# Kernel optimization log

Hardware: AMD Instinct MI355X
Metric: run time of the kernel (lower is better)

Reference implementation:

```python
import jax, jax.numpy as jnp
import numpy as np

B = 8192      # batch
D = 512       # ode state dim = 4*h_dim
U = 100       # ode net hidden units
K_STEPS = 20  # opt.ode1_step
EPS = 0.01    # opt.ode2_eps


def setup_inputs() -> dict:
    key = jax.random.key(0)
    ks = jax.random.split(key, 12)
    std = 0.1  # init_network_weights std
    return {
        "y0": jax.random.normal(ks[0], (B, D), jnp.float32),
        "t_seq": jax.random.uniform(ks[1], (B, 2), dtype=jnp.float32),
        "W1": std * jax.random.normal(ks[2], (U, D), jnp.float32),
        "b1": jnp.zeros((U,), jnp.float32),
        "W2": std * jax.random.normal(ks[3], (U, U), jnp.float32),
        "b2": jnp.zeros((U,), jnp.float32),
        "W3": std * jax.random.normal(ks[4], (D, U), jnp.float32),
        "b3": jnp.zeros((D,), jnp.float32),
        "b_phi_zt": jax.random.normal(ks[5], (B, 1), jnp.float32),
        # derivative of Nonpositive net is <= 0; log(-b' + 0.01) requires b' < 0.01
        "b_phi_zt_deriv": -jax.random.uniform(ks[6], (B, 1), dtype=jnp.float32),
        "s_phi_zt": jax.random.normal(ks[7], (B, 1), jnp.float32),
        "s_phi_zt_deriv": jax.random.uniform(ks[8], (B, 1), dtype=jnp.float32),
        "k": K_STEPS,
    }


def _ode_net(y, W1, b1, W2, b2, W3, b3):
    # create_net(D, D, n_layers=1, n_units=U): Linear->Tanh->Linear->Tanh->Linear
    h = jnp.tanh(y @ W1.T + b1)
    h = jnp.tanh(h @ W2.T + b2)
    return h @ W3.T + b3


def _forward(y0, t_seq, W1, b1, W2, b2, W3, b3,
             b_phi_zt, b_phi_zt_deriv, s_phi_zt, s_phi_zt_deriv, k):
    # ---- DiffeqSolver: k fixed Euler steps, gradient net ignores t ----
    dt = (t_seq[:, 1:2] - t_seq[:, 0:1]) / k  # [B,1]

    def euler_step(yi, _):
        yi = yi + _ode_net(yi, W1, b1, W2, b2, W3, b3) * dt
        return yi, None

    y_final, _ = jax.lax.scan(euler_step, y0, None, length=k)

    # ---- DiffeqSolver_KL: y_t = y0 + eps * cumsum(g(m_t)); y0 = 0 ----
    const = 0.01
    Kv = s_phi_zt + jnp.log(-b_phi_zt_deriv + const) - jnp.log(s_phi_zt_deriv + const)  # [B,1]
    T = int(round(1.0 / EPS)) - 1  # steps t = 1 .. int(1/eps)-1
    ms = (-1.0 + EPS * jnp.arange(1, T + 1, dtype=jnp.float32))[:, None, None]  # [T,1,1]
    log_neg_m = jnp.log(-ms)
    gm = -b_phi_zt_deriv / (ms * log_neg_m) * (Kv - jnp.log(-log_neg_m))  # [T,B,1]
    ycum = EPS * jnp.cumsum(gm, axis=0)  # solutions[t-1] = ycum[t-1]
    loss = ycum[-1] + (ycum[-2] - ycum[-1])  # first_item + Gm_eps  -> [B,1]

    return jnp.concatenate([y_final, loss], axis=-1)  # [B, D+1]


def reference(y0, t_seq, W1, b1, W2, b2, W3, b3,
              b_phi_zt, b_phi_zt_deriv, s_phi_zt, s_phi_zt_deriv, k):
    return _forward(y0, t_seq, W1, b1, W2, b2, W3, b3,
                    b_phi_zt, b_phi_zt_deriv, s_phi_zt, s_phi_zt_deriv, k)
```

## Files before the change

kernel.cpp:

```cpp
#include <hip/hip_runtime.h>


typedef __attribute__((ext_vector_type(8))) short s16x8;
typedef __attribute__((ext_vector_type(4))) float fx4;

#define NB 8192
#define DD 512
#define UU 100
#define UP 128
#define BM 32

__device__ __forceinline__ unsigned int f2bf(float x) {
  unsigned int u = __float_as_uint(x);
  return (u + 0x7FFFu + ((u >> 16) & 1u)) >> 16;
}
__device__ __forceinline__ float bf2f(unsigned int h) {
  return __uint_as_float(h << 16);
}
__device__ __forceinline__ unsigned int cvt_pk_bf16(float lo, float hi) {
  unsigned int r;
  asm("v_cvt_pk_bf16_f32 %0, %1, %2" : "=v"(r) : "v"(lo), "v"(hi));
  return r;
}
__device__ __forceinline__ float tanh5(float x) {
  float e = __builtin_amdgcn_exp2f(x * 2.885390081777927f);
  return 1.0f - 2.0f / (e + 1.0f);
}

__global__ void prep_weights(const float* __restrict__ W1,
                             const float* __restrict__ W2,
                             const float* __restrict__ W3,
                             const float* __restrict__ b2,
                             const float* __restrict__ b3,
                             unsigned short* __restrict__ ws) {
  int e = blockIdx.x * 256 + threadIdx.x;
  if (e < 65536) {
    int u = e >> 9, kc = e & 511;
    ws[e] = (u < UU) ? (unsigned short)f2bf(W1[u * DD + kc]) : (unsigned short)0;
  } else if (e < 81920) {
    int e2 = e - 65536;
    int n = e2 >> 7, kc = e2 & 127;
    unsigned short v = 0;
    if (kc == 127)      v = (n < UU) ? (unsigned short)f2bf(b2[n]) : (unsigned short)0;
    else if (n < UU && kc < UU) v = (unsigned short)f2bf(W2[n * UU + kc]);
    ws[e] = v;
  } else if (e < 147456) {
    int e3 = e - 81920;
    int d = e3 >> 7, kc = e3 & 127;
    unsigned short v = 0;
    if (kc == 127)      v = (unsigned short)f2bf(b3[d]);
    else if (kc < UU)   v = (unsigned short)f2bf(W3[d * UU + kc]);
    ws[e] = v;
  }
}

__global__ __launch_bounds__(512) __attribute__((amdgpu_waves_per_eu(2, 2)))
void ode_main(
    const float* __restrict__ y0, const float* __restrict__ t_seq,
    const float* __restrict__ b1,
    const unsigned short* __restrict__ W1b,
    const unsigned short* __restrict__ W2b,
    const unsigned short* __restrict__ W3b,
    const int* __restrict__ kptr, float* __restrict__ out) {
  __shared__ char Yb[BM * DD * 2];
  __shared__ char H1[BM * UP * 2];
  __shared__ char H2[BM * UP * 2];

  const int tid  = threadIdx.x;
  const int w    = tid >> 6;
  const int lane = tid & 63;
  const int lo   = lane & 15;
  const int hi   = lane >> 4;
  const int b0   = blockIdx.x * BM;
  const int k    = *kptr;
  const float kinv = 1.0f / (float)k;

  auto ybo = [](int b, int byr) -> int { return (b << 10) + (byr ^ ((b & 7) << 4)); };
  auto ho  = [](int b, int byr) -> int { return (b << 8)  + (byr ^ ((b & 7) << 4)); };

  s16x8 w1r[16];
#pragma unroll
  for (int kk = 0; kk < 16; ++kk)
    w1r[kk] = *(const s16x8*)(W1b + (16 * w + lo) * DD + kk * 32 + hi * 8);
  s16x8 w2r[4];
#pragma unroll
  for (int kk = 0; kk < 4; ++kk)
    w2r[kk] = *(const s16x8*)(W2b + (16 * w + lo) * UP + kk * 32 + hi * 8);
  s16x8 w3r[4][4];
#pragma unroll
  for (int i = 0; i < 4; ++i)
#pragma unroll
    for (int kk = 0; kk < 4; ++kk)
      w3r[i][kk] = *(const s16x8*)(W3b + ((4 * w + i) * 16 + lo) * UP + kk * 32 + hi * 8);

  float b1v[4];
#pragma unroll
  for (int r = 0; r < 4; ++r) {
    int u = 16 * w + 4 * hi + r;
    b1v[r] = (u < UU) ? b1[u] : 0.0f;
  }
  float dt2[2];
#pragma unroll
  for (int j = 0; j < 2; ++j) {
    int b = b0 + j * 16 + lo;
    dt2[j] = (t_seq[2 * b + 1] - t_seq[2 * b]) * kinv;
  }

  fx4 Yr[4][2];
#pragma unroll
  for (int i = 0; i < 4; ++i)
#pragma unroll
    for (int j = 0; j < 2; ++j) {
      const float* p = y0 + (size_t)(b0 + j * 16 + lo) * DD + (4 * w + i) * 16 + hi * 4;
      Yr[i][j] = *(const fx4*)p;
    }

  auto write_yb = [&]() {
#pragma unroll
    for (int i = 0; i < 4; ++i)
#pragma unroll
      for (int j = 0; j < 2; ++j) {
        uint2 q;
        q.x = cvt_pk_bf16(Yr[i][j][0], Yr[i][j][1]);
        q.y = cvt_pk_bf16(Yr[i][j][2], Yr[i][j][3]);
        *(uint2*)(Yb + ybo(j * 16 + lo, ((4 * w + i) * 16 + hi * 4) * 2)) = q;
      }
  };
  write_yb();
  __syncthreads();

  const fx4 zf = {0.f, 0.f, 0.f, 0.f};

#pragma unroll 1
  for (int s = 0; s < k; ++s) {
    {
      fx4 aA[2], aB[2];
#pragma unroll
      for (int j = 0; j < 2; ++j)
#pragma unroll
        for (int r = 0; r < 4; ++r) { aA[j][r] = b1v[r]; aB[j][r] = 0.0f; }
      __builtin_amdgcn_s_setprio(1);
#pragma unroll
      for (int kk = 0; kk < 16; kk += 2) {
        int bro0 = kk * 64 + hi * 16;
        int bro1 = (kk + 1) * 64 + hi * 16;
        s16x8 b00 = *(const s16x8*)(Yb + ybo(lo, bro0));
        s16x8 b01 = *(const s16x8*)(Yb + ybo(16 + lo, bro0));
        s16x8 b10 = *(const s16x8*)(Yb + ybo(lo, bro1));
        s16x8 b11 = *(const s16x8*)(Yb + ybo(16 + lo, bro1));
        aA[0] = __builtin_amdgcn_mfma_f32_16x16x32_bf16(w1r[kk], b00, aA[0], 0, 0, 0);
        aA[1] = __builtin_amdgcn_mfma_f32_16x16x32_bf16(w1r[kk], b01, aA[1], 0, 0, 0);
        aB[0] = __builtin_amdgcn_mfma_f32_16x16x32_bf16(w1r[kk + 1], b10, aB[0], 0, 0, 0);
        aB[1] = __builtin_amdgcn_mfma_f32_16x16x32_bf16(w1r[kk + 1], b11, aB[1], 0, 0, 0);
      }
      __builtin_amdgcn_s_setprio(0);
#pragma unroll
      for (int j = 0; j < 2; ++j) {
        float v0 = tanh5(aA[j][0] + aB[j][0]);
        float v1 = tanh5(aA[j][1] + aB[j][1]);
        float v2 = tanh5(aA[j][2] + aB[j][2]);
        float v3 = tanh5(aA[j][3] + aB[j][3]);
        if (w == 7 && hi == 3) v3 = 1.0f;
        uint2 q;
        q.x = cvt_pk_bf16(v0, v1);
        q.y = cvt_pk_bf16(v2, v3);
        *(uint2*)(H1 + ho(j * 16 + lo, (16 * w + 4 * hi) * 2)) = q;
      }
    }
    __syncthreads();

    {
      fx4 c2[2];
      c2[0] = zf; c2[1] = zf;
      __builtin_amdgcn_s_setprio(1);
#pragma unroll
      for (int kk = 0; kk < 4; ++kk) {
        int bro = kk * 64 + hi * 16;
        s16x8 hb0 = *(const s16x8*)(H1 + ho(lo, bro));
        s16x8 hb1 = *(const s16x8*)(H1 + ho(16 + lo, bro));
        c2[0] = __builtin_amdgcn_mfma_f32_16x16x32_bf16(w2r[kk], hb0, c2[0], 0, 0, 0);
        c2[1] = __builtin_amdgcn_mfma_f32_16x16x32_bf16(w2r[kk], hb1, c2[1], 0, 0, 0);
      }
      __builtin_amdgcn_s_setprio(0);
#pragma unroll
      for (int j = 0; j < 2; ++j) {
        float h0 = tanh5(c2[j][0]) * dt2[j];
        float h1x = tanh5(c2[j][1]) * dt2[j];
        float h2x = tanh5(c2[j][2]) * dt2[j];
        float h3 = tanh5(c2[j][3]) * dt2[j];
        if (w == 7 && hi == 3) h3 = dt2[j];
        uint2 q;
        q.x = cvt_pk_bf16(h0, h1x);
        q.y = cvt_pk_bf16(h2x, h3);
        *(uint2*)(H2 + ho(j * 16 + lo, (16 * w + 4 * hi) * 2)) = q;
      }
    }
    __syncthreads();

    __builtin_amdgcn_s_setprio(1);
#pragma unroll
    for (int kk = 0; kk < 4; ++kk) {
      int bro = kk * 64 + hi * 16;
      s16x8 bb0 = *(const s16x8*)(H2 + ho(lo, bro));
      s16x8 bb1 = *(const s16x8*)(H2 + ho(16 + lo, bro));
#pragma unroll
      for (int i = 0; i < 4; ++i) {
        Yr[i][0] = __builtin_amdgcn_mfma_f32_16x16x32_bf16(w3r[i][kk], bb0, Yr[i][0], 0, 0, 0);
        Yr[i][1] = __builtin_amdgcn_mfma_f32_16x16x32_bf16(w3r[i][kk], bb1, Yr[i][1], 0, 0, 0);
      }
    }
    __builtin_amdgcn_s_setprio(0);
    write_yb();
    __syncthreads();
  }

  for (int idx = tid; idx < BM * DD; idx += 512) {
    int b = idx >> 9, d = idx & 511;
    unsigned short hx = *(const unsigned short*)(Yb + ybo(b, 2 * d));
    out[(size_t)(b0 + b) * 513 + d] = bf2f((unsigned int)hx);
  }
}

__global__ void loss_kernel(const float* __restrict__ bdp,
                            const float* __restrict__ sp,
                            const float* __restrict__ sdp,
                            float* __restrict__ out) {
  int b = blockIdx.x * 256 + threadIdx.x;
  if (b >= NB) return;
  float bd = bdp[b];
  float Kv = sp[b] + __logf(-bd + 0.01f) - __logf(sdp[b] + 0.01f);
  float acc = 0.0f;
  for (int t = 1; t <= 98; ++t) {
    float m = 0.01f * (float)t - 1.0f;
    float L = __logf(-m);
    acc += (-bd) / (m * L) * (Kv - __logf(-L));
  }
  out[(size_t)b * 513 + 512] = 0.01f * acc;
}

extern "C" void kernel_launch(void* const* d_in, const int* in_sizes, int n_in,
                              void* d_out, int out_size, void* d_ws, size_t ws_size,
                              hipStream_t stream) {
  const float* y0    = (const float*)d_in[0];
  const float* t_seq = (const float*)d_in[1];
  const float* W1    = (const float*)d_in[2];
  const float* b1    = (const float*)d_in[3];
  const float* W2    = (const float*)d_in[4];
  const float* b2    = (const float*)d_in[5];
  const float* W3    = (const float*)d_in[6];
  const float* b3    = (const float*)d_in[7];
  const float* bd    = (const float*)d_in[9];
  const float* s_    = (const float*)d_in[10];
  const float* sd    = (const float*)d_in[11];
  const int*   kptr  = (const int*)d_in[12];
  float* out = (float*)d_out;
  unsigned short* ws = (unsigned short*)d_ws;

  prep_weights<<<576, 256, 0, stream>>>(W1, W2, W3, b2, b3, ws);
  ode_main<<<256, 512, 0, stream>>>(y0, t_seq, b1,
                                    ws, ws + 65536, ws + 81920, kptr, out);
  loss_kernel<<<32, 256, 0, stream>>>(bd, s_, sd, out);
}
```

Baseline: 94.26 us.

## Replace XOR-swizzled LDS layout with padded strides and pin MFMA weights in AGPRs

Replaces the XOR-swizzle addressing of the Y, H1 and H2 shared-memory tiles with padded row strides (1040 and 272 bytes), so read and write addresses become per-thread base offsets plus compile-time constants. This removes per-access index arithmetic and is meant to keep LDS bank conflicts low. It also routes every MFMA through inline asm that forces the A operand (the weight fragments) into AGPRs, relieving VGPR pressure at 2 waves per EU. Costs are a little extra LDS for the padding, and the inline asm hides the MFMAs from the compiler scheduler, which can hurt instruction interleaving.

```diff
diff --git a/kernel.cpp b/kernel.cpp
--- a/kernel.cpp
+++ b/kernel.cpp
@@ -9,6 +9,8 @@
 #define UU 100
 #define UP 128
 #define BM 32
+#define YSTR 1040
+#define HSTR 272
 
 __device__ __forceinline__ unsigned int f2bf(float x) {
   unsigned int u = __float_as_uint(x);
@@ -25,6 +27,10 @@
 __device__ __forceinline__ float tanh5(float x) {
   float e = __builtin_amdgcn_exp2f(x * 2.885390081777927f);
   return 1.0f - 2.0f / (e + 1.0f);
+}
+__device__ __forceinline__ fx4 mfma_a(s16x8 a, s16x8 b, fx4 c) {
+  asm("v_mfma_f32_16x16x32_bf16 %0, %1, %2, %0" : "+v"(c) : "a"(a), "v"(b));
+  return c;
 }
 
 __global__ void prep_weights(const float* __restrict__ W1,
@@ -62,9 +68,9 @@
     const unsigned short* __restrict__ W2b,
     const unsigned short* __restrict__ W3b,
     const int* __restrict__ kptr, float* __restrict__ out) {
-  __shared__ char Yb[BM * DD * 2];
-  __shared__ char H1[BM * UP * 2];
-  __shared__ char H2[BM * UP * 2];
+  __shared__ char Yb[BM * YSTR];
+  __shared__ char H1[BM * HSTR];
+  __shared__ char H2[BM * HSTR];
 
   const int tid  = threadIdx.x;
   const int w    = tid >> 6;
@@ -75,8 +81,10 @@
   const int k    = *kptr;
   const float kinv = 1.0f / (float)k;
 
-  auto ybo = [](int b, int byr) -> int { return (b << 10) + (byr ^ ((b & 7) << 4)); };
-  auto ho  = [](int b, int byr) -> int { return (b << 8)  + (byr ^ ((b & 7) << 4)); };
+  const int yrb  = lo * YSTR + hi * 16;
+  const int ywb  = lo * YSTR + w * 128 + hi * 8;
+  const int hrb  = lo * HSTR + hi * 16;
+  const int hwb  = lo * HSTR + w * 32 + hi * 8;
 
   s16x8 w1r[16];
 #pragma unroll
@@ -123,7 +131,7 @@
         uint2 q;
         q.x = cvt_pk_bf16(Yr[i][j][0], Yr[i][j][1]);
         q.y = cvt_pk_bf16(Yr[i][j][2], Yr[i][j][3]);
-        *(uint2*)(Yb + ybo(j * 16 + lo, ((4 * w + i) * 16 + hi * 4) * 2)) = q;
+        *(uint2*)(Yb + ywb + i * 32 + j * 16 * YSTR) = q;
       }
   };
   write_yb();
@@ -142,16 +150,14 @@
       __builtin_amdgcn_s_setprio(1);
 #pragma unroll
       for (int kk = 0; kk < 16; kk += 2) {
-        int bro0 = kk * 64 + hi * 16;
-        int bro1 = (kk + 1) * 64 + hi * 16;
-        s16x8 b00 = *(const s16x8*)(Yb + ybo(lo, bro0));
-        s16x8 b01 = *(const s16x8*)(Yb + ybo(16 + lo, bro0));
-        s16x8 b10 = *(const s16x8*)(Yb + ybo(lo, bro1));
-        s16x8 b11 = *(const s16x8*)(Yb + ybo(16 + lo, bro1));
-        aA[0] = __builtin_amdgcn_mfma_f32_16x16x32_bf16(w1r[kk], b00, aA[0], 0, 0, 0);
-        aA[1] = __builtin_amdgcn_mfma_f32_16x16x32_bf16(w1r[kk], b01, aA[1], 0, 0, 0);
-        aB[0] = __builtin_amdgcn_mfma_f32_16x16x32_bf16(w1r[kk + 1], b10, aB[0], 0, 0, 0);
-        aB[1] = __builtin_amdgcn_mfma_f32_16x16x32_bf16(w1r[kk + 1], b11, aB[1], 0, 0, 0);
+        s16x8 b00 = *(const s16x8*)(Yb + yrb + kk * 64);
+        s16x8 b01 = *(const s16x8*)(Yb + yrb + kk * 64 + 16 * YSTR);
+        s16x8 b10 = *(const s16x8*)(Yb + yrb + (kk + 1) * 64);
+        s16x8 b11 = *(const s16x8*)(Yb + yrb + (kk + 1) * 64 + 16 * YSTR);
+        aA[0] = mfma_a(w1r[kk], b00, aA[0]);
+        aA[1] = mfma_a(w1r[kk], b01, aA[1]);
+        aB[0] = mfma_a(w1r[kk + 1], b10, aB[0]);
+        aB[1] = mfma_a(w1r[kk + 1], b11, aB[1]);
       }
       __builtin_amdgcn_s_setprio(0);
 #pragma unroll
@@ -164,7 +170,7 @@
         uint2 q;
         q.x = cvt_pk_bf16(v0, v1);
         q.y = cvt_pk_bf16(v2, v3);
-        *(uint2*)(H1 + ho(j * 16 + lo, (16 * w + 4 * hi) * 2)) = q;
+        *(uint2*)(H1 + hwb + j * 16 * HSTR) = q;
       }
     }
     __syncthreads();
@@ -175,11 +181,10 @@
       __builtin_amdgcn_s_setprio(1);
 #pragma unroll
       for (int kk = 0; kk < 4; ++kk) {
-        int bro = kk * 64 + hi * 16;
-        s16x8 hb0 = *(const s16x8*)(H1 + ho(lo, bro));
-        s16x8 hb1 = *(const s16x8*)(H1 + ho(16 + lo, bro));
-        c2[0] = __builtin_amdgcn_mfma_f32_16x16x32_bf16(w2r[kk], hb0, c2[0], 0, 0, 0);
-        c2[1] = __builtin_amdgcn_mfma_f32_16x16x32_bf16(w2r[kk], hb1, c2[1], 0, 0, 0);
+        s16x8 hb0 = *(const s16x8*)(H1 + hrb + kk * 64);
+        s16x8 hb1 = *(const s16x8*)(H1 + hrb + kk * 64 + 16 * HSTR);
+        c2[0] = mfma_a(w2r[kk], hb0, c2[0]);
+        c2[1] = mfma_a(w2r[kk], hb1, c2[1]);
       }
       __builtin_amdgcn_s_setprio(0);
 #pragma unroll
@@ -192,7 +197,7 @@
         uint2 q;
         q.x = cvt_pk_bf16(h0, h1x);
         q.y = cvt_pk_bf16(h2x, h3);
-        *(uint2*)(H2 + ho(j * 16 + lo, (16 * w + 4 * hi) * 2)) = q;
+        *(uint2*)(H2 + hwb + j * 16 * HSTR) = q;
       }
     }
     __syncthreads();
@@ -200,13 +205,12 @@
     __builtin_amdgcn_s_setprio(1);
 #pragma unroll
     for (int kk = 0; kk < 4; ++kk) {
-      int bro = kk * 64 + hi * 16;
-      s16x8 bb0 = *(const s16x8*)(H2 + ho(lo, bro));
-      s16x8 bb1 = *(const s16x8*)(H2 + ho(16 + lo, bro));
+      s16x8 bb0 = *(const s16x8*)(H2 + hrb + kk * 64);
+      s16x8 bb1 = *(const s16x8*)(H2 + hrb + kk * 64 + 16 * HSTR);
 #pragma unroll
       for (int i = 0; i < 4; ++i) {
-        Yr[i][0] = __builtin_amdgcn_mfma_f32_16x16x32_bf16(w3r[i][kk], bb0, Yr[i][0], 0, 0, 0);
-        Yr[i][1] = __builtin_amdgcn_mfma_f32_16x16x32_bf16(w3r[i][kk], bb1, Yr[i][1], 0, 0, 0);
+        Yr[i][0] = mfma_a(w3r[i][kk], bb0, Yr[i][0]);
+        Yr[i][1] = mfma_a(w3r[i][kk], bb1, Yr[i][1]);
       }
     }
     __builtin_amdgcn_s_setprio(0);
@@ -216,7 +220,7 @@
 
   for (int idx = tid; idx < BM * DD; idx += 512) {
     int b = idx >> 9, d = idx & 511;
-    unsigned short hx = *(const unsigned short*)(Yb + ybo(b, 2 * d));
+    unsigned short hx = *(const unsigned short*)(Yb + b * YSTR + 2 * d);
     out[(size_t)(b0 + b) * 513 + d] = bf2f((unsigned int)hx);
   }
 }
```

After: 93.09 us. About the same (-1.2%).
